# Kernel optimization log

Measured on AMD Instinct MI355X. Metric: run time of the kernel, lower is better.

Reference implementation:

```python
import jax, jax.numpy as jnp
import numpy as np

B = 1024          # batch
L = 200           # max_len (history length)
DIM = 64          # args.dim
ITEM_NUM = 100000 # vocab; table has ITEM_NUM+1 rows, row 0 = padding
NEG = -1e15       # mask additive constant used by the original module


def setup_inputs() -> dict:
    key = jax.random.key(0)
    k1, k2, k3, k4, k5 = jax.random.split(key, 5)
    log_seqs = jax.random.randint(k1, (B, L), 0, ITEM_NUM + 1)          # item ids, 0 = pad
    pred = jax.random.randint(k2, (B, 1), 0, ITEM_NUM + 1)              # gather targets
    item_emb = jax.random.normal(k3, (ITEM_NUM + 1, DIM), jnp.float32) * 0.02
    item_emb = item_emb.at[0].set(0.0)                                  # padding_idx=0
    attn_key = jax.random.uniform(k4, (1, DIM), jnp.float32)            # self.key (torch.rand init)
    pos_emb = jax.random.normal(k5, (L, DIM), jnp.float32) * 0.02       # positional table
    return {"log_seqs": log_seqs, "pred": pred, "item_emb": item_emb,
            "attn_key": attn_key, "pos_emb": pos_emb}


def reference(log_seqs, pred, item_emb, attn_key, pos_emb):
    dim = item_emb.shape[1]
    mask = log_seqs != 0                                  # [B, L] True where valid
    # log2feats (model='P2MAMO', dropout p=0 -> identity)
    seqs = item_emb[log_seqs] * jnp.sqrt(jnp.float32(dim))  # [B, L, D]
    seqs = seqs + pos_emb[None, :, :]
    seqs = seqs * mask[..., None]                         # zero out padded positions
    # single-query dot-product attention pooling with learned key
    sim = jnp.einsum('bld,d->bl', seqs, attn_key[0])      # (q*k).sum(-1)
    sim = sim + jnp.where(mask, 0.0, NEG)                 # sim + (~mask)*-1e15
    attn = jax.nn.softmax(sim, axis=-1)                   # [B, L]
    Q = jnp.einsum('bld,bl->bd', seqs, attn)              # [B, D]
    # training path (isEval=False): full-vocab logits -> softmax -> gather
    logits = Q @ item_emb.T                               # [B, V+1]
    probs = jax.nn.softmax(logits, axis=-1)
    pos_logits = jnp.take_along_axis(probs, pred, axis=1) # [B, 1]
    return pos_logits
```

## Files before the change

### kernel.cpp

```cpp
#include <hip/hip_runtime.h>
#include <math.h>

#define B_TOT   1024
#define L_SEQ   200
#define DIM     64
#define VOCAB   100001
#define NEG_BIG (-1e15f)
#define SEQ_STRIDE 68

typedef __bf16 bf16x8 __attribute__((ext_vector_type(8)));
typedef float  f32x4  __attribute__((ext_vector_type(4)));

__global__ __launch_bounds__(256) void pool_kernel(
    const int*   __restrict__ log_seqs,
    const float* __restrict__ item_emb,
    const float* __restrict__ attn_key,
    const float* __restrict__ pos_emb,
    float*       __restrict__ Q,
    __bf16*      __restrict__ Qb,
    __bf16*      __restrict__ Eb)
{
    const int b    = blockIdx.x;
    const int t    = threadIdx.x;
    const int wave = t >> 6;
    const int lane = t & 63;

    __shared__ float s_seq[L_SEQ][SEQ_STRIDE];
    __shared__ float s_attn[L_SEQ];
    __shared__ float s_red[4];
    __shared__ float s_q[4][DIM];

    {
        const long n8 = ((long)VOCAB * DIM) / 8;
        for (long g = (long)b * 256 + t; g < n8; g += (long)gridDim.x * 256) {
            const long i = g * 8;
            const float4 f0 = ((const float4*)(item_emb + i))[0];
            const float4 f1 = ((const float4*)(item_emb + i))[1];
            bf16x8 o;
            o[0] = (__bf16)f0.x; o[1] = (__bf16)f0.y; o[2] = (__bf16)f0.z; o[3] = (__bf16)f0.w;
            o[4] = (__bf16)f1.x; o[5] = (__bf16)f1.y; o[6] = (__bf16)f1.z; o[7] = (__bf16)f1.w;
            *(bf16x8*)(Eb + i) = o;
        }
    }

    float sim = -INFINITY;
    if (t < L_SEQ) {
        const int id = log_seqs[(long)b * L_SEQ + t];
        if (id == 0) {
            sim = NEG_BIG;
            #pragma unroll
            for (int i = 0; i < DIM / 4; ++i)
                *(float4*)(&s_seq[t][4 * i]) = make_float4(0.f, 0.f, 0.f, 0.f);
        } else {
            float acc = 0.f;
            const float4* e4 = (const float4*)(item_emb + (long)id * DIM);
            const float4* p4 = (const float4*)(pos_emb + t * DIM);
            #pragma unroll
            for (int i = 0; i < DIM / 4; ++i) {
                const float4 e = e4[i];
                const float4 p = p4[i];
                float4 f;
                f.x = fmaf(8.f, e.x, p.x);
                f.y = fmaf(8.f, e.y, p.y);
                f.z = fmaf(8.f, e.z, p.z);
                f.w = fmaf(8.f, e.w, p.w);
                *(float4*)(&s_seq[t][4 * i]) = f;
                acc += f.x * attn_key[4*i+0] + f.y * attn_key[4*i+1]
                     + f.z * attn_key[4*i+2] + f.w * attn_key[4*i+3];
            }
            sim = acc;
        }
    }

    float m = sim;
    #pragma unroll
    for (int off = 32; off > 0; off >>= 1) m = fmaxf(m, __shfl_xor(m, off));
    if (lane == 0) s_red[wave] = m;
    __syncthreads();
    m = fmaxf(fmaxf(s_red[0], s_red[1]), fmaxf(s_red[2], s_red[3]));
    __syncthreads();

    float p = (t < L_SEQ) ? __expf(sim - m) : 0.f;
    if (t < L_SEQ) s_attn[t] = p;
    float ls = p;
    #pragma unroll
    for (int off = 32; off > 0; off >>= 1) ls += __shfl_xor(ls, off);
    if (lane == 0) s_red[wave] = ls;
    __syncthreads();
    const float inv = 1.0f / (s_red[0] + s_red[1] + s_red[2] + s_red[3]);

    float q = 0.f;
    const int l0 = wave * (L_SEQ / 4);
    #pragma unroll 2
    for (int l = l0; l < l0 + (L_SEQ / 4); ++l)
        q = fmaf(s_attn[l], s_seq[l][lane], q);
    s_q[wave][lane] = q;
    __syncthreads();

    if (t < DIM) {
        const float qq = (s_q[0][t] + s_q[1][t] + s_q[2][t] + s_q[3][t]) * inv;
        Q[b * DIM + t]  = qq;
        Qb[b * DIM + t] = (__bf16)qq;
    }
}

#define NC        64
#define NBG       8
#define VT_TOTAL  6251
#define VT_FULL   6250

__global__ __launch_bounds__(256) void logits_mfma(
    const __bf16* __restrict__ Eb,
    const __bf16* __restrict__ Qb,
    float*        __restrict__ partials)
{
    const int bid   = blockIdx.x;
    const int xcd   = bid & 7;
    const int idx   = bid >> 3;
    const int chunk = xcd + 8 * (idx >> 3);
    const int bg    = idx & 7;
    const int wave  = threadIdx.x >> 6;
    const int lane  = threadIdx.x & 63;
    const int r16   = lane & 15;
    const int hi    = lane >> 4;

    bf16x8 a[8][2];
    #pragma unroll
    for (int t = 0; t < 8; ++t)
        #pragma unroll
        for (int s = 0; s < 2; ++s)
            a[t][s] = *(const bf16x8*)(Qb + ((bg*128 + t*16 + r16) * DIM) + s*32 + hi*8);

    const int per    = (VT_TOTAL + NC - 1) / NC;
    const int vt_end = min((chunk + 1) * per, VT_TOTAL);
    int vt = chunk * per + wave;

    float ssum[8][4];
    #pragma unroll
    for (int t = 0; t < 8; ++t)
        #pragma unroll
        for (int r = 0; r < 4; ++r) ssum[t][r] = 0.f;

    bf16x8 b0, b1;
    if (vt < vt_end) {
        const int row = min(vt * 16 + r16, VOCAB - 1);
        const __bf16* p = Eb + (size_t)row * DIM + hi * 8;
        b0 = *(const bf16x8*)p;
        b1 = *(const bf16x8*)(p + 32);
    }
    while (vt < vt_end) {
        const bf16x8 c0 = b0, c1 = b1;
        const int vt_cur = vt;
        vt += 4;
        if (vt < vt_end) {
            const int row = min(vt * 16 + r16, VOCAB - 1);
            const __bf16* p = Eb + (size_t)row * DIM + hi * 8;
            b0 = *(const bf16x8*)p;
            b1 = *(const bf16x8*)(p + 32);
        }
        if (vt_cur < VT_FULL) {
            #pragma unroll
            for (int t = 0; t < 8; ++t) {
                f32x4 acc = {0.f, 0.f, 0.f, 0.f};
                acc = __builtin_amdgcn_mfma_f32_16x16x32_bf16(a[t][0], c0, acc, 0, 0, 0);
                acc = __builtin_amdgcn_mfma_f32_16x16x32_bf16(a[t][1], c1, acc, 0, 0, 0);
                #pragma unroll
                for (int r = 0; r < 4; ++r) ssum[t][r] += __expf(acc[r]);
            }
        } else {
            const bool valid = (vt_cur * 16 + r16) < VOCAB;
            #pragma unroll
            for (int t = 0; t < 8; ++t) {
                f32x4 acc = {0.f, 0.f, 0.f, 0.f};
                acc = __builtin_amdgcn_mfma_f32_16x16x32_bf16(a[t][0], c0, acc, 0, 0, 0);
                acc = __builtin_amdgcn_mfma_f32_16x16x32_bf16(a[t][1], c1, acc, 0, 0, 0);
                #pragma unroll
                for (int r = 0; r < 4; ++r) ssum[t][r] += valid ? __expf(acc[r]) : 0.f;
            }
        }
    }

    #pragma unroll
    for (int t = 0; t < 8; ++t)
        #pragma unroll
        for (int r = 0; r < 4; ++r) {
            float v = ssum[t][r];
            v += __shfl_xor(v, 1);
            v += __shfl_xor(v, 2);
            v += __shfl_xor(v, 4);
            v += __shfl_xor(v, 8);
            ssum[t][r] = v;
        }

    if (r16 == 0) {
        const int wslot = chunk * 4 + wave;
        #pragma unroll
        for (int t = 0; t < 8; ++t)
            #pragma unroll
            for (int r = 0; r < 4; ++r) {
                const int row = bg * 128 + t * 16 + hi * 4 + r;
                partials[(size_t)wslot * B_TOT + row] = ssum[t][r];
            }
    }
}

__global__ __launch_bounds__(256) void finalize_kernel(
    const float* __restrict__ Q,
    const float* __restrict__ item_emb,
    const int*   __restrict__ pred,
    const float* __restrict__ partials,
    float*       __restrict__ out)
{
    const int b = blockIdx.x * 256 + threadIdx.x;

    float S = 0.f;
    for (int w = 0; w < NC * 4; ++w)
        S += partials[(size_t)w * B_TOT + b];

    const int pv = pred[b];
    float acc = 0.f;
    const float4* e4 = (const float4*)(item_emb + (long)pv * DIM);
    const float4* q4 = (const float4*)(Q + b * DIM);
    #pragma unroll
    for (int i = 0; i < DIM / 4; ++i) {
        const float4 e = e4[i];
        const float4 q = q4[i];
        acc += e.x*q.x + e.y*q.y + e.z*q.z + e.w*q.w;
    }
    out[b] = __expf(acc) / S;
}

extern "C" void kernel_launch(void* const* d_in, const int* in_sizes, int n_in,
                              void* d_out, int out_size, void* d_ws, size_t ws_size,
                              hipStream_t stream)
{
    const int*   log_seqs = (const int*)  d_in[0];
    const int*   pred     = (const int*)  d_in[1];
    const float* item_emb = (const float*)d_in[2];
    const float* attn_key = (const float*)d_in[3];
    const float* pos_emb  = (const float*)d_in[4];
    float*       out      = (float*)d_out;

    char* ws = (char*)d_ws;
    __bf16* Eb       = (__bf16*)ws;
    __bf16* Qb       = (__bf16*)(ws + (size_t)VOCAB * DIM * 2);
    float*  Qf       = (float*) (ws + (size_t)VOCAB * DIM * 2 + (size_t)B_TOT * DIM * 2);
    float*  partials = (float*) ((char*)Qf + (size_t)B_TOT * DIM * 4);

    pool_kernel<<<B_TOT, 256, 0, stream>>>(log_seqs, item_emb, attn_key, pos_emb, Qf, Qb, Eb);
    logits_mfma<<<NBG * NC, 256, 0, stream>>>(Eb, Qb, partials);
    finalize_kernel<<<B_TOT / 256, 256, 0, stream>>>(Qf, item_emb, pred, partials, out);
}
```

Before: 69.88 us.

## Double vocab chunks, prefetch two tiles ahead, reduce partials in LDS

```diff
diff --git a/kernel.cpp b/kernel.cpp
--- a/kernel.cpp
+++ b/kernel.cpp
@@ -104,7 +104,7 @@
     }
 }
 
-#define NC        64
+#define NC        128
 #define NBG       8
 #define VT_TOTAL  6251
 #define VT_FULL   6250
@@ -124,6 +124,8 @@
     const int r16   = lane & 15;
     const int hi    = lane >> 4;
 
+    __shared__ float s_part[4][128];
+
     bf16x8 a[8][2];
     #pragma unroll
     for (int t = 0; t < 8; ++t)
@@ -141,44 +143,68 @@
         #pragma unroll
         for (int r = 0; r < 4; ++r) ssum[t][r] = 0.f;
 
-    bf16x8 b0, b1;
-    if (vt < vt_end) {
-        const int row = min(vt * 16 + r16, VOCAB - 1);
-        const __bf16* p = Eb + (size_t)row * DIM + hi * 8;
-        b0 = *(const bf16x8*)p;
-        b1 = *(const bf16x8*)(p + 32);
-    }
+    #define LOADB(dst0, dst1, vti) do {                                       \
+        const int _row = min((vti) * 16 + r16, VOCAB - 1);                    \
+        const __bf16* _p = Eb + (size_t)_row * DIM + hi * 8;                  \
+        dst0 = *(const bf16x8*)_p;                                            \
+        dst1 = *(const bf16x8*)(_p + 32);                                     \
+    } while (0)
+
+    bf16x8 b0, b1, d0, d1;
+    LOADB(b0, b1, vt);
+    LOADB(d0, d1, vt + 4);
+
     while (vt < vt_end) {
-        const bf16x8 c0 = b0, c1 = b1;
-        const int vt_cur = vt;
-        vt += 4;
-        if (vt < vt_end) {
-            const int row = min(vt * 16 + r16, VOCAB - 1);
-            const __bf16* p = Eb + (size_t)row * DIM + hi * 8;
-            b0 = *(const bf16x8*)p;
-            b1 = *(const bf16x8*)(p + 32);
-        }
-        if (vt_cur < VT_FULL) {
+        const bf16x8 c00 = b0, c01 = b1, c10 = d0, c11 = d1;
+        const int v0 = vt, v1 = vt + 4;
+        vt += 8;
+        LOADB(b0, b1, vt);
+        LOADB(d0, d1, vt + 4);
+
+        if (v0 < VT_FULL) {
             #pragma unroll
             for (int t = 0; t < 8; ++t) {
                 f32x4 acc = {0.f, 0.f, 0.f, 0.f};
-                acc = __builtin_amdgcn_mfma_f32_16x16x32_bf16(a[t][0], c0, acc, 0, 0, 0);
-                acc = __builtin_amdgcn_mfma_f32_16x16x32_bf16(a[t][1], c1, acc, 0, 0, 0);
+                acc = __builtin_amdgcn_mfma_f32_16x16x32_bf16(a[t][0], c00, acc, 0, 0, 0);
+                acc = __builtin_amdgcn_mfma_f32_16x16x32_bf16(a[t][1], c01, acc, 0, 0, 0);
                 #pragma unroll
                 for (int r = 0; r < 4; ++r) ssum[t][r] += __expf(acc[r]);
             }
         } else {
-            const bool valid = (vt_cur * 16 + r16) < VOCAB;
+            const bool valid = (v0 * 16 + r16) < VOCAB;
             #pragma unroll
             for (int t = 0; t < 8; ++t) {
                 f32x4 acc = {0.f, 0.f, 0.f, 0.f};
-                acc = __builtin_amdgcn_mfma_f32_16x16x32_bf16(a[t][0], c0, acc, 0, 0, 0);
-                acc = __builtin_amdgcn_mfma_f32_16x16x32_bf16(a[t][1], c1, acc, 0, 0, 0);
+                acc = __builtin_amdgcn_mfma_f32_16x16x32_bf16(a[t][0], c00, acc, 0, 0, 0);
+                acc = __builtin_amdgcn_mfma_f32_16x16x32_bf16(a[t][1], c01, acc, 0, 0, 0);
                 #pragma unroll
                 for (int r = 0; r < 4; ++r) ssum[t][r] += valid ? __expf(acc[r]) : 0.f;
             }
         }
-    }
+        if (v1 < vt_end) {
+            if (v1 < VT_FULL) {
+                #pragma unroll
+                for (int t = 0; t < 8; ++t) {
+                    f32x4 acc = {0.f, 0.f, 0.f, 0.f};
+                    acc = __builtin_amdgcn_mfma_f32_16x16x32_bf16(a[t][0], c10, acc, 0, 0, 0);
+                    acc = __builtin_amdgcn_mfma_f32_16x16x32_bf16(a[t][1], c11, acc, 0, 0, 0);
+                    #pragma unroll
+                    for (int r = 0; r < 4; ++r) ssum[t][r] += __expf(acc[r]);
+                }
+            } else {
+                const bool valid = (v1 * 16 + r16) < VOCAB;
+                #pragma unroll
+                for (int t = 0; t < 8; ++t) {
+                    f32x4 acc = {0.f, 0.f, 0.f, 0.f};
+                    acc = __builtin_amdgcn_mfma_f32_16x16x32_bf16(a[t][0], c10, acc, 0, 0, 0);
+                    acc = __builtin_amdgcn_mfma_f32_16x16x32_bf16(a[t][1], c11, acc, 0, 0, 0);
+                    #pragma unroll
+                    for (int r = 0; r < 4; ++r) ssum[t][r] += valid ? __expf(acc[r]) : 0.f;
+                }
+            }
+        }
+    }
+    #undef LOADB
 
     #pragma unroll
     for (int t = 0; t < 8; ++t)
@@ -193,14 +219,18 @@
         }
 
     if (r16 == 0) {
-        const int wslot = chunk * 4 + wave;
         #pragma unroll
         for (int t = 0; t < 8; ++t)
             #pragma unroll
-            for (int r = 0; r < 4; ++r) {
-                const int row = bg * 128 + t * 16 + hi * 4 + r;
-                partials[(size_t)wslot * B_TOT + row] = ssum[t][r];
-            }
+            for (int r = 0; r < 4; ++r)
+                s_part[wave][t * 16 + hi * 4 + r] = ssum[t][r];
+    }
+    __syncthreads();
+
+    if (threadIdx.x < 128) {
+        const int i = threadIdx.x;
+        const float v = s_part[0][i] + s_part[1][i] + s_part[2][i] + s_part[3][i];
+        partials[(size_t)chunk * B_TOT + bg * 128 + i] = v;
     }
 }
 
@@ -214,8 +244,8 @@
     const int b = blockIdx.x * 256 + threadIdx.x;
 
     float S = 0.f;
-    for (int w = 0; w < NC * 4; ++w)
-        S += partials[(size_t)w * B_TOT + b];
+    for (int c = 0; c < NC; ++c)
+        S += partials[(size_t)c * B_TOT + b];
 
     const int pv = pred[b];
     float acc = 0.f;
```

New measurement: 68.60 us. Within noise of the previous version (-1.8%).
